# Kernel tuning notes

Measured on AMD Instinct MI355X. Metric: run time of the kernel, lower is better.

Reference implementation:

```python
import jax, jax.numpy as jnp
import numpy as np

B, C, E, H = 8, 2048, 1024, 128


def setup_inputs() -> dict:
    key = jax.random.key(0)
    kx, kq, kk, kv = jax.random.split(key, 4)
    scale = 1.0 / np.sqrt(E)
    return {
        "x": jax.random.normal(kx, (B, C, E), dtype=jnp.float32),
        "Wq": jax.random.normal(kq, (E, H), dtype=jnp.float32) * scale,
        "Wk": jax.random.normal(kk, (E, H), dtype=jnp.float32) * scale,
        "Wv": jax.random.normal(kv, (E, H), dtype=jnp.float32) * scale,
    }


def reference(x, Wq, Wk, Wv):
    # x: (B, C, E); projections -> (B, C, H)
    q = jnp.einsum("bce,eh->bch", x, Wq)
    k = jnp.einsum("bce,eh->bch", x, Wk)
    v = jnp.einsum("bce,eh->bch", x, Wv)
    # NOTE: original scales by sqrt(embed_size), not head_size
    scores = jnp.einsum("bqh,bkh->bqk", q, k) / jnp.sqrt(jnp.asarray(E, x.dtype))
    Cq = x.shape[1]
    causal = jnp.tril(jnp.ones((Cq, Cq), dtype=bool))
    scores = jnp.where(causal, scores, -jnp.inf)
    weights = jax.nn.softmax(scores, axis=-1)  # (B, C, C)
    out = jnp.einsum("bqk,bkh->bqh", weights, v)
    return out
```

## Files before the change

kernel.cpp:

```cpp
#include <hip/hip_runtime.h>
#include <hip/hip_bf16.h>

#define BATCH 8
#define CTX   2048
#define EMB   1024
#define HD    128
#define VSTR  2080

using bf16x8 = __attribute__((ext_vector_type(8))) short;
using fx4    = __attribute__((ext_vector_type(4))) float;

__device__ __forceinline__ ushort f2bf(float f) {
    union { float f; unsigned u; } v; v.f = f;
    unsigned u = v.u;
    u += 0x7fffu + ((u >> 16) & 1u);
    return (ushort)(u >> 16);
}

__device__ __forceinline__ unsigned cvtpk(float a, float b) {
    unsigned r;
    asm("v_cvt_pk_bf16_f32 %0, %1, %2" : "=v"(r) : "v"(a), "v"(b));
    return r;
}

__device__ __forceinline__ void gload16(const void* g, void* l) {
    __builtin_amdgcn_global_load_lds(
        (const __attribute__((address_space(1))) unsigned*)g,
        (__attribute__((address_space(3))) unsigned*)l, 16, 0, 0);
}

__global__ void wt_kernel(const float* __restrict__ Wq, const float* __restrict__ Wk,
                          const float* __restrict__ Wv, ushort* __restrict__ Wt) {
    int idx = blockIdx.x * blockDim.x + threadIdx.x;
    int e = idx % EMB;
    int h = (idx / EMB) % HD;
    int w = idx / (EMB * HD);
    const float* W = (w == 0) ? Wq : (w == 1) ? Wk : Wv;
    Wt[idx] = f2bf(W[e * HD + h]);
}

__global__ __launch_bounds__(256) void proj_kernel(
        const float* __restrict__ x, const ushort* __restrict__ Wt,
        ushort* __restrict__ q, ushort* __restrict__ k, ushort* __restrict__ vt) {
    __shared__ __align__(16) float  As[32 * 64];
    __shared__ __align__(16) ushort Bs[192 * 64];

    const int t    = threadIdx.x;
    const int wave = t >> 6;
    const int lane = t & 63;
    const int lo = lane & 15, hi = lane >> 4;
    const int brow = blockIdx.x * 32;
    const int bcol = blockIdx.y * 192;

    const char* Ab = (const char*)As;
    const char* Bb = (const char*)Bs;

    fx4 acc[2][3];
#pragma unroll
    for (int m2 = 0; m2 < 2; m2++)
#pragma unroll
        for (int n = 0; n < 3; n++) acc[m2][n] = fx4{0.f, 0.f, 0.f, 0.f};

    const int arow_s = t >> 4;
    const int acol_s = ((t & 15) ^ (arow_s & 7)) << 2;
    const int brow_s = t >> 3;
    const int bcol_s = ((t & 7) ^ (brow_s & 7)) << 3;
    const int ldsbase = wave * 1024;

    for (int k0 = 0; k0 < EMB; k0 += 64) {
#pragma unroll
        for (int r = 0; r < 2; r++)
            gload16(x + (size_t)(brow + r * 16 + arow_s) * EMB + k0 + acol_s,
                    (char*)As + r * 4096 + ldsbase);
#pragma unroll
        for (int r = 0; r < 6; r++)
            gload16(Wt + (size_t)(bcol + r * 32 + brow_s) * EMB + k0 + bcol_s,
                    (char*)Bs + r * 4096 + ldsbase);
        __syncthreads();

#pragma unroll
        for (int ks = 0; ks < 2; ks++) {
            bf16x8 af[2], bfr[3];
#pragma unroll
            for (int m2 = 0; m2 < 2; m2++) {
                const int rowA = m2 * 16 + lo;
                const unsigned sw = (rowA & 7) << 4;
                const unsigned ub = rowA * 256 + ks * 128 + hi * 32;
                fx4 a0 = *(const fx4*)(Ab + (ub ^ sw));
                fx4 a1 = *(const fx4*)(Ab + ((ub + 16) ^ sw));
                union { unsigned u[4]; bf16x8 v; } pk;
                pk.u[0] = cvtpk(a0[0], a0[1]);
                pk.u[1] = cvtpk(a0[2], a0[3]);
                pk.u[2] = cvtpk(a1[0], a1[1]);
                pk.u[3] = cvtpk(a1[2], a1[3]);
                af[m2] = pk.v;
            }
#pragma unroll
            for (int n = 0; n < 3; n++) {
                const int rowB = wave * 48 + n * 16 + lo;
                const unsigned ub = rowB * 128 + ks * 64 + hi * 16;
                bfr[n] = *(const bf16x8*)(Bb + (ub ^ ((rowB & 7) << 4)));
            }
#pragma unroll
            for (int m2 = 0; m2 < 2; m2++)
#pragma unroll
                for (int n = 0; n < 3; n++)
                    acc[m2][n] = __builtin_amdgcn_mfma_f32_16x16x32_bf16(af[m2], bfr[n], acc[m2][n], 0, 0, 0);
        }
        __syncthreads();
    }

    const float qscale = 0.03125f;
#pragma unroll
    for (int n = 0; n < 3; n++) {
        const int col = bcol + wave * 48 + n * 16 + lo;
        const int bnn = col >> 7;
        const int cc  = col & 127;
#pragma unroll
        for (int m2 = 0; m2 < 2; m2++) {
#pragma unroll
            for (int j = 0; j < 4; j++) {
                const int r = brow + m2 * 16 + hi * 4 + j;
                if (bnn == 0)      q[(size_t)r * HD + cc] = f2bf(acc[m2][n][j] * qscale);
                else if (bnn == 1) k[(size_t)r * HD + cc] = f2bf(acc[m2][n][j]);
                else {
                    const int bb2 = r >> 11, ccc = r & (CTX - 1);
                    vt[((size_t)bb2 * HD + cc) * VSTR + ccc] = f2bf(acc[m2][n][j]);
                }
            }
        }
    }
}

__global__ __launch_bounds__(256) void attn_kernel(
        const ushort* __restrict__ q, const ushort* __restrict__ k,
        const ushort* __restrict__ vt, float* __restrict__ out) {
    __shared__ __align__(16) char Ks[2][16384];
    __shared__ __align__(16) char Vs[2][16384];
    __shared__ __align__(16) char p_lds[4][1024];

    const int id   = blockIdx.x;
    const int b    = id & 7;
    const int pos  = id >> 3;
    const int qt   = (pos < 32) ? (63 - pos) : (pos - 32);
    const int t    = threadIdx.x;
    const int wave = t >> 6;
    const int lane = t & 63;
    const int lo = lane & 15, hi = lane >> 4;
    const int wq = wave & 1, w = wave >> 1;
    const int q0 = qt * 32 + wq * 16;

    const ushort* qb = q  + (size_t)b * CTX * HD;
    const ushort* kb = k  + (size_t)b * CTX * HD;
    const ushort* vb = vt + (size_t)b * HD * VSTR;

    bf16x8 qf[4];
#pragma unroll
    for (int ks = 0; ks < 4; ks++)
        qf[ks] = *(const bf16x8*)(qb + (q0 + lo) * HD + ks * 32 + hi * 8);

    fx4 o[8];
#pragma unroll
    for (int h = 0; h < 8; h++) o[h] = fx4{0.f, 0.f, 0.f, 0.f};
    float m[4], l[4];
#pragma unroll
    for (int j = 0; j < 4; j++) { m[j] = 0.f; l[j] = 0.f; }

#define STAGE(bi, kv0_) do {                                                   \
    _Pragma("unroll")                                                          \
    for (int r = 0; r < 4; ++r) {                                              \
        const int row = r * 16 + (t >> 4);                                     \
        gload16(kb + (size_t)((kv0_) + row) * HD + (((t & 15) ^ (row & 7)) << 3), \
                Ks[bi] + r * 4096 + wave * 1024);                              \
    }                                                                          \
    _Pragma("unroll")                                                          \
    for (int r = 0; r < 4; ++r) {                                              \
        const int row = r * 32 + (t >> 3);                                     \
        gload16(vb + (size_t)row * VSTR + (kv0_) + (((t & 7) ^ (row & 7)) << 3), \
                Vs[bi] + r * 4096 + wave * 1024);                              \
    }                                                                          \
} while (0)

    const int nkv = qt / 2 + 1;
    STAGE(0, 0);
    for (int it = 0; it < nkv; ++it) {
        asm volatile("s_waitcnt vmcnt(0)" ::: "memory");
        __builtin_amdgcn_sched_barrier(0);
        __builtin_amdgcn_s_barrier();
        __builtin_amdgcn_sched_barrier(0);
        if (it + 1 < nkv) STAGE((it + 1) & 1, (it + 1) * 64);

        const char* Kb = Ks[it & 1];
        const char* Vb = Vs[it & 1];
        const int kv0 = it * 64;

        fx4 s[2];
        s[0] = fx4{0.f, 0.f, 0.f, 0.f};
        s[1] = fx4{0.f, 0.f, 0.f, 0.f};
        __builtin_amdgcn_s_setprio(1);
#pragma unroll
        for (int n2 = 0; n2 < 2; n2++) {
            const int row = w * 32 + n2 * 16 + lo;
            const unsigned sw = (unsigned)((row & 7) << 4);
#pragma unroll
            for (int ks = 0; ks < 4; ks++) {
                bf16x8 kf = *(const bf16x8*)(Kb + row * 256 + ((ks * 64 + hi * 16) ^ sw));
                s[n2] = __builtin_amdgcn_mfma_f32_16x16x32_bf16(qf[ks], kf, s[n2], 0, 0, 0);
            }
        }
        __builtin_amdgcn_s_setprio(0);

        const bool diag = (kv0 + 64 > q0);
        float pmax[4];
        int allok = 1;
#pragma unroll
        for (int j = 0; j < 4; j++) {
            const int r = q0 + hi * 4 + j;
            if (diag) {
#pragma unroll
                for (int n2 = 0; n2 < 2; n2++)
                    if ((kv0 + w * 32 + n2 * 16 + lo) > r) s[n2][j] = -INFINITY;
            }
            pmax[j] = fmaxf(s[0][j], s[1][j]);
            allok &= (pmax[j] <= m[j] + 16.0f);
        }
        if (!__all(allok)) {
#pragma unroll
            for (int j = 0; j < 4; j++) {
                float mx = pmax[j];
                mx = fmaxf(mx, __shfl_xor(mx, 1));
                mx = fmaxf(mx, __shfl_xor(mx, 2));
                mx = fmaxf(mx, __shfl_xor(mx, 4));
                mx = fmaxf(mx, __shfl_xor(mx, 8));
                const float mn = fmaxf(m[j], mx);
                const float f  = __expf(m[j] - mn);
                l[j] *= f;
#pragma unroll
                for (int h = 0; h < 8; h++) o[h][j] *= f;
                m[j] = mn;
            }
        }
#pragma unroll
        for (int j = 0; j < 4; j++) {
            float sum = 0.f;
#pragma unroll
            for (int n2 = 0; n2 < 2; n2++) {
                const float pv = __expf(s[n2][j] - m[j]);
                s[n2][j] = pv;
                sum += pv;
            }
            l[j] += sum;
            const int row = hi * 4 + j;
            const unsigned sw = (unsigned)((row & 3) << 4);
#pragma unroll
            for (int n2 = 0; n2 < 2; n2++) {
                const unsigned cb = (unsigned)((n2 * 16 + lo) * 2);
                *(ushort*)(p_lds[wave] + row * 64 + (cb ^ sw)) = f2bf(s[n2][j]);
            }
        }
        asm volatile("" ::: "memory");
        bf16x8 pa = *(const bf16x8*)(p_lds[wave] + lo * 64 + ((hi * 16) ^ ((lo & 3) << 4)));
        __builtin_amdgcn_s_setprio(1);
#pragma unroll
        for (int h = 0; h < 8; h++) {
            const int vr = h * 16 + lo;
            bf16x8 vf = *(const bf16x8*)(Vb + vr * 128 + ((w * 64 + hi * 16) ^ ((vr & 7) << 4)));
            o[h] = __builtin_amdgcn_mfma_f32_16x16x32_bf16(pa, vf, o[h], 0, 0, 0);
        }
        __builtin_amdgcn_s_setprio(0);
    }
#undef STAGE

#pragma unroll
    for (int j = 0; j < 4; j++) {
        l[j] += __shfl_xor(l[j], 1);
        l[j] += __shfl_xor(l[j], 2);
        l[j] += __shfl_xor(l[j], 4);
        l[j] += __shfl_xor(l[j], 8);
    }

    float* oB  = (float*)Ks[0];
    float* mlB = (float*)Vs[0];
    __syncthreads();
    if (w == 1) {
#pragma unroll
        for (int j = 0; j < 4; j++) {
            const int row = hi * 4 + j;
            if (lo == 0) { mlB[wq * 32 + row] = m[j]; mlB[wq * 32 + 16 + row] = l[j]; }
#pragma unroll
            for (int h = 0; h < 8; h++)
                oB[(wq * 16 + row) * 128 + h * 16 + lo] = o[h][j];
        }
    }
    __syncthreads();
    if (w == 0) {
        float* ob = out + ((size_t)b * CTX + q0) * HD;
#pragma unroll
        for (int j = 0; j < 4; j++) {
            const int row = hi * 4 + j;
            const float mB = mlB[wq * 32 + row], lB = mlB[wq * 32 + 16 + row];
            const float mt = fmaxf(m[j], mB);
            const float fA = __expf(m[j] - mt);
            const float fB = __expf(mB - mt);
            const float inv = 1.0f / (l[j] * fA + lB * fB);
#pragma unroll
            for (int h = 0; h < 8; h++)
                ob[row * HD + h * 16 + lo] =
                    (o[h][j] * fA + oB[(wq * 16 + row) * 128 + h * 16 + lo] * fB) * inv;
        }
    }
}

extern "C" void kernel_launch(void* const* d_in, const int* in_sizes, int n_in,
                              void* d_out, int out_size, void* d_ws, size_t ws_size,
                              hipStream_t stream) {
    const float* x  = (const float*)d_in[0];
    const float* Wq = (const float*)d_in[1];
    const float* Wk = (const float*)d_in[2];
    const float* Wv = (const float*)d_in[3];

    ushort* Wt = (ushort*)d_ws;
    ushort* qw = (ushort*)((char*)d_ws + 786432);
    ushort* kw = qw + (size_t)BATCH * CTX * HD;
    ushort* vw = kw + (size_t)BATCH * CTX * HD;

    wt_kernel<<<(3 * HD * EMB) / 256, 256, 0, stream>>>(Wq, Wk, Wv, Wt);
    proj_kernel<<<dim3(512, 2), 256, 0, stream>>>(x, Wt, qw, kw, vw);
    attn_kernel<<<512, 256, 0, stream>>>(qw, kw, vw, (float*)d_out);
}
```

Baseline: 90.27 us.

## Restructure attention into 16-row query blocks with direct V register loads and exp2 softmax

The attention kernel is split into 1024 two-wave blocks of 16 query rows instead of 512 four-wave blocks of 32 rows. V tiles are now loaded straight from global memory into registers, so only K is staged in LDS. The K rows are interleaved so the probability tile can be packed with cvt_pk and written to LDS without swizzling. The softmax uses a raw v_exp_f32 (exp2) with the log2(e) factor folded into the Q scale. The changes are meant to cut LDS traffic and footprint and to raise occupancy, at the cost of more global loads of V per query row and a barrier each iteration.

```diff
diff --git a/kernel.cpp b/kernel.cpp
--- a/kernel.cpp
+++ b/kernel.cpp
@@ -20,6 +20,12 @@
 __device__ __forceinline__ unsigned cvtpk(float a, float b) {
     unsigned r;
     asm("v_cvt_pk_bf16_f32 %0, %1, %2" : "=v"(r) : "v"(a), "v"(b));
+    return r;
+}
+
+__device__ __forceinline__ float exp2a(float x) {
+    float r;
+    asm("v_exp_f32 %0, %1" : "=v"(r) : "v"(x));
     return r;
 }
 
@@ -110,7 +116,7 @@
         __syncthreads();
     }
 
-    const float qscale = 0.03125f;
+    const float qscale = 0.045084219f;
 #pragma unroll
     for (int n = 0; n < 3; n++) {
         const int col = bcol + wave * 48 + n * 16 + lo;
@@ -132,23 +138,21 @@
     }
 }
 
-__global__ __launch_bounds__(256) void attn_kernel(
+__global__ __launch_bounds__(128) void attn_kernel(
         const ushort* __restrict__ q, const ushort* __restrict__ k,
         const ushort* __restrict__ vt, float* __restrict__ out) {
     __shared__ __align__(16) char Ks[2][16384];
-    __shared__ __align__(16) char Vs[2][16384];
-    __shared__ __align__(16) char p_lds[4][1024];
+    __shared__ __align__(16) char p_lds[2][1024];
 
     const int id   = blockIdx.x;
     const int b    = id & 7;
     const int pos  = id >> 3;
-    const int qt   = (pos < 32) ? (63 - pos) : (pos - 32);
+    const int qt   = (pos < 64) ? (127 - pos) : (pos - 64);
+    const int q0   = qt * 16;
     const int t    = threadIdx.x;
-    const int wave = t >> 6;
+    const int w    = t >> 6;
     const int lane = t & 63;
     const int lo = lane & 15, hi = lane >> 4;
-    const int wq = wave & 1, w = wave >> 1;
-    const int q0 = qt * 32 + wq * 16;
 
     const ushort* qb = q  + (size_t)b * CTX * HD;
     const ushort* kb = k  + (size_t)b * CTX * HD;
@@ -166,45 +170,43 @@
 #pragma unroll
     for (int j = 0; j < 4; j++) { m[j] = 0.f; l[j] = 0.f; }
 
-#define STAGE(bi, kv0_) do {                                                   \
+    const int krow = t >> 4;
+
+#define KSTAGE(bi, kv0_) do {                                                  \
     _Pragma("unroll")                                                          \
-    for (int r = 0; r < 4; ++r) {                                              \
-        const int row = r * 16 + (t >> 4);                                     \
-        gload16(kb + (size_t)((kv0_) + row) * HD + (((t & 15) ^ (row & 7)) << 3), \
-                Ks[bi] + r * 4096 + wave * 1024);                              \
-    }                                                                          \
-    _Pragma("unroll")                                                          \
-    for (int r = 0; r < 4; ++r) {                                              \
-        const int row = r * 32 + (t >> 3);                                     \
-        gload16(vb + (size_t)row * VSTR + (kv0_) + (((t & 7) ^ (row & 7)) << 3), \
-                Vs[bi] + r * 4096 + wave * 1024);                              \
+    for (int r = 0; r < 8; ++r) {                                              \
+        const int key = ((r * 4) + (krow >> 1)) & 7;                           \
+        gload16(kb + (size_t)((kv0_) + r * 8 + krow) * HD + (((t & 15) ^ key) << 3), \
+                Ks[bi] + r * 2048 + w * 1024);                                 \
     }                                                                          \
 } while (0)
 
-    const int nkv = qt / 2 + 1;
-    STAGE(0, 0);
+    const int nkv = qt / 4 + 1;
+    KSTAGE(0, 0);
+    asm volatile("s_waitcnt vmcnt(0)" ::: "memory");
+    __builtin_amdgcn_sched_barrier(0);
+    __builtin_amdgcn_s_barrier();
+    __builtin_amdgcn_sched_barrier(0);
+
     for (int it = 0; it < nkv; ++it) {
-        asm volatile("s_waitcnt vmcnt(0)" ::: "memory");
-        __builtin_amdgcn_sched_barrier(0);
-        __builtin_amdgcn_s_barrier();
-        __builtin_amdgcn_sched_barrier(0);
-        if (it + 1 < nkv) STAGE((it + 1) & 1, (it + 1) * 64);
+        const int kv0 = it * 64;
+        bf16x8 vf[8];
+#pragma unroll
+        for (int h = 0; h < 8; h++)
+            vf[h] = *(const bf16x8*)(vb + (size_t)(h * 16 + lo) * VSTR + kv0 + w * 32 + hi * 8);
+        if (it + 1 < nkv) KSTAGE((it + 1) & 1, kv0 + 64);
 
         const char* Kb = Ks[it & 1];
-        const char* Vb = Vs[it & 1];
-        const int kv0 = it * 64;
-
         fx4 s[2];
         s[0] = fx4{0.f, 0.f, 0.f, 0.f};
         s[1] = fx4{0.f, 0.f, 0.f, 0.f};
         __builtin_amdgcn_s_setprio(1);
 #pragma unroll
         for (int n2 = 0; n2 < 2; n2++) {
-            const int row = w * 32 + n2 * 16 + lo;
-            const unsigned sw = (unsigned)((row & 7) << 4);
+            const int row = w * 32 + 2 * lo + n2;
 #pragma unroll
             for (int ks = 0; ks < 4; ks++) {
-                bf16x8 kf = *(const bf16x8*)(Kb + row * 256 + ((ks * 64 + hi * 16) ^ sw));
+                bf16x8 kf = *(const bf16x8*)(Kb + row * 256 + ((ks * 64 + hi * 16) ^ ((lo & 7) << 4)));
                 s[n2] = __builtin_amdgcn_mfma_f32_16x16x32_bf16(qf[ks], kf, s[n2], 0, 0, 0);
             }
         }
@@ -217,12 +219,12 @@
         for (int j = 0; j < 4; j++) {
             const int r = q0 + hi * 4 + j;
             if (diag) {
-#pragma unroll
-                for (int n2 = 0; n2 < 2; n2++)
-                    if ((kv0 + w * 32 + n2 * 16 + lo) > r) s[n2][j] = -INFINITY;
+                const int c0 = kv0 + w * 32 + 2 * lo;
+                if (c0 > r)     s[0][j] = -INFINITY;
+                if (c0 + 1 > r) s[1][j] = -INFINITY;
             }
             pmax[j] = fmaxf(s[0][j], s[1][j]);
-            allok &= (pmax[j] <= m[j] + 16.0f);
+            allok &= (pmax[j] <= m[j] + 23.0f);
         }
         if (!__all(allok)) {
 #pragma unroll
@@ -233,7 +235,7 @@
                 mx = fmaxf(mx, __shfl_xor(mx, 4));
                 mx = fmaxf(mx, __shfl_xor(mx, 8));
                 const float mn = fmaxf(m[j], mx);
-                const float f  = __expf(m[j] - mn);
+                const float f  = exp2a(m[j] - mn);
                 l[j] *= f;
 #pragma unroll
                 for (int h = 0; h < 8; h++) o[h][j] *= f;
@@ -242,34 +244,25 @@
         }
 #pragma unroll
         for (int j = 0; j < 4; j++) {
-            float sum = 0.f;
-#pragma unroll
-            for (int n2 = 0; n2 < 2; n2++) {
-                const float pv = __expf(s[n2][j] - m[j]);
-                s[n2][j] = pv;
-                sum += pv;
-            }
-            l[j] += sum;
-            const int row = hi * 4 + j;
-            const unsigned sw = (unsigned)((row & 3) << 4);
-#pragma unroll
-            for (int n2 = 0; n2 < 2; n2++) {
-                const unsigned cb = (unsigned)((n2 * 16 + lo) * 2);
-                *(ushort*)(p_lds[wave] + row * 64 + (cb ^ sw)) = f2bf(s[n2][j]);
-            }
+            const float p0 = exp2a(s[0][j] - m[j]);
+            const float p1 = exp2a(s[1][j] - m[j]);
+            l[j] += p0 + p1;
+            *(unsigned*)(p_lds[w] + (hi * 4 + j) * 64 + lo * 4) = cvtpk(p0, p1);
         }
         asm volatile("" ::: "memory");
-        bf16x8 pa = *(const bf16x8*)(p_lds[wave] + lo * 64 + ((hi * 16) ^ ((lo & 3) << 4)));
+        bf16x8 pa = *(const bf16x8*)(p_lds[w] + lo * 64 + hi * 16);
         __builtin_amdgcn_s_setprio(1);
 #pragma unroll
-        for (int h = 0; h < 8; h++) {
-            const int vr = h * 16 + lo;
-            bf16x8 vf = *(const bf16x8*)(Vb + vr * 128 + ((w * 64 + hi * 16) ^ ((vr & 7) << 4)));
-            o[h] = __builtin_amdgcn_mfma_f32_16x16x32_bf16(pa, vf, o[h], 0, 0, 0);
-        }
+        for (int h = 0; h < 8; h++)
+            o[h] = __builtin_amdgcn_mfma_f32_16x16x32_bf16(pa, vf[h], o[h], 0, 0, 0);
         __builtin_amdgcn_s_setprio(0);
-    }
-#undef STAGE
+
+        asm volatile("s_waitcnt vmcnt(0)" ::: "memory");
+        __builtin_amdgcn_sched_barrier(0);
+        __builtin_amdgcn_s_barrier();
+        __builtin_amdgcn_sched_barrier(0);
+    }
+#undef KSTAGE
 
 #pragma unroll
     for (int j = 0; j < 4; j++) {
@@ -280,16 +273,15 @@
     }
 
     float* oB  = (float*)Ks[0];
-    float* mlB = (float*)Vs[0];
+    float* mlB = (float*)Ks[1];
     __syncthreads();
     if (w == 1) {
 #pragma unroll
         for (int j = 0; j < 4; j++) {
             const int row = hi * 4 + j;
-            if (lo == 0) { mlB[wq * 32 + row] = m[j]; mlB[wq * 32 + 16 + row] = l[j]; }
-#pragma unroll
-            for (int h = 0; h < 8; h++)
-                oB[(wq * 16 + row) * 128 + h * 16 + lo] = o[h][j];
+            if (lo == 0) { mlB[row] = m[j]; mlB[16 + row] = l[j]; }
+#pragma unroll
+            for (int h = 0; h < 8; h++) oB[row * 128 + h * 16 + lo] = o[h][j];
         }
     }
     __syncthreads();
@@ -298,15 +290,15 @@
 #pragma unroll
         for (int j = 0; j < 4; j++) {
             const int row = hi * 4 + j;
-            const float mB = mlB[wq * 32 + row], lB = mlB[wq * 32 + 16 + row];
+            const float mB = mlB[row], lB = mlB[16 + row];
             const float mt = fmaxf(m[j], mB);
-            const float fA = __expf(m[j] - mt);
-            const float fB = __expf(mB - mt);
+            const float fA = exp2a(m[j] - mt);
+            const float fB = exp2a(mB - mt);
             const float inv = 1.0f / (l[j] * fA + lB * fB);
 #pragma unroll
             for (int h = 0; h < 8; h++)
                 ob[row * HD + h * 16 + lo] =
-                    (o[h][j] * fA + oB[(wq * 16 + row) * 128 + h * 16 + lo] * fB) * inv;
+                    (o[h][j] * fA + oB[row * 128 + h * 16 + lo] * fB) * inv;
         }
     }
 }
@@ -326,5 +318,5 @@
 
     wt_kernel<<<(3 * HD * EMB) / 256, 256, 0, stream>>>(Wq, Wk, Wv, Wt);
     proj_kernel<<<dim3(512, 2), 256, 0, stream>>>(x, Wt, qw, kw, vw);
-    attn_kernel<<<512, 256, 0, stream>>>(qw, kw, vw, (float*)d_out);
-}
+    attn_kernel<<<1024, 128, 0, stream>>>(qw, kw, vw, (float*)d_out);
+}
```

Measured after the change: 90.50 us. Within noise of the previous version (+0.3%).
